# Kernel tuning notes

Hardware: AMD Instinct MI355X
Metric: run time of the kernel (lower is better)

The kernel has to match this reference:

```python
import jax, jax.numpy as jnp
import numpy as np

B, N, F = 1048576, 20, 7
RADIUS = 0.15
L1, L2 = 0.1, 2.0


def setup_inputs() -> dict:
    key = jax.random.key(0)
    ks = jax.random.split(key, 8)
    half = N // 2
    return {
        "x": jax.random.normal(ks[0], (B, N, F), dtype=jnp.float32),
        "W1": jax.random.normal(ks[1], (39, 64), dtype=jnp.float32) * 0.1,
        "b1": jax.random.normal(ks[2], (64,), dtype=jnp.float32) * 0.1,
        "W2": jax.random.normal(ks[3], (64, 64), dtype=jnp.float32) * 0.1,
        "b2": jax.random.normal(ks[4], (64,), dtype=jnp.float32) * 0.1,
        "W3": jax.random.normal(ks[5], (64, 5), dtype=jnp.float32) * 0.1,
        "b3": jax.random.normal(ks[6], (5,), dtype=jnp.float32) * 0.1,
        "idx": jax.random.randint(ks[7], (8,), 0, half, dtype=jnp.int32),
    }


def _build_observation(x, idx):
    # x: [B, N, 7]; agent_index = 0 (init kwarg)
    agent_index = 0
    half = N // 2
    Bsz = x.shape[0]
    pos = x[:, agent_index, 0:2]                      # [B,2]
    o_self = x[:, agent_index, 0:5]                   # [B,5]

    # three random agent neighbors: rel goal-like quantity, then a zero column
    xi = x[:, idx[0:3], :]                            # [B,3,7]
    rel = xi[..., 5:7] + xi[..., 0:2] - pos[:, None]  # [B,3,2]
    mid = jnp.concatenate(
        [rel, jnp.zeros((Bsz, 3, 1), dtype=x.dtype)], axis=2
    ).reshape(Bsz, 9)

    # five random obstacles (second half): distance-masked relative pos + features
    jdx = idx[3:8] + half
    xo = x[:, jdx, :]                                 # [B,5,7]
    d = xo[..., 0:2] - pos[:, None]                   # [B,5,2]
    dist = jnp.linalg.norm(d, axis=-1)                # [B,5]
    mask = (dist < RADIUS)[..., None]                 # [B,5,1]
    a = jnp.where(mask, d, 0.0)                       # [B,5,2]
    f = jnp.where(mask, xo[..., 2:5], 0.0)            # [B,5,3]
    obst = jnp.concatenate([a, f], axis=2).reshape(Bsz, 25)

    return jnp.concatenate([o_self, mid, obst], axis=1)  # [B,39]


def reference(x, W1, b1, W2, b2, W3, b3, idx):
    obs = _build_observation(x, idx)
    h = jax.nn.relu(obs @ W1 + b1)
    h = jax.nn.relu(h @ W2 + b2)
    r = h @ W3 + b3                                   # [B,5]
    res = jnp.stack([r[:, 1] - r[:, 2], r[:, 3] - r[:, 4]], axis=1) * L1
    res = jnp.where(jnp.abs(res) > 1.0, jnp.sign(res) * L2, res)
    return res
```

## Files before the change

### kernel.cpp

```cpp
#include <hip/hip_runtime.h>
#include <math.h>


#define NROW 20
#define NF   7
#define ITEM_F (NROW * NF)
#define BLOCK 128

__global__ __launch_bounds__(BLOCK) void maddpg_kernel(
    const float* __restrict__ x,
    const float* __restrict__ W1, const float* __restrict__ b1,
    const float* __restrict__ W2, const float* __restrict__ b2,
    const float* __restrict__ W3, const float* __restrict__ b3,
    const int*   __restrict__ idx,
    float2*      __restrict__ out,
    int nitems)
{
    __shared__ float buf[64 * BLOCK];

    const int tid = threadIdx.x;
    const long b  = (long)blockIdx.x * BLOCK + tid;
    if (b >= nitems) return;

    const float* xb = x + b * (long)ITEM_F;

    float4 s0 = *(const float4*)(xb);
    float  s4 = xb[4];
    const float px = s0.x, py = s0.y;
    buf[0*BLOCK + tid] = s0.x;
    buf[1*BLOCK + tid] = s0.y;
    buf[2*BLOCK + tid] = s0.z;
    buf[3*BLOCK + tid] = s0.w;
    buf[4*BLOCK + tid] = s4;

    #pragma unroll
    for (int t = 0; t < 3; t++) {
        const float* xr = xb + idx[t] * NF;
        float2 p01 = *(const float2*)(xr);
        float2 p56 = *(const float2*)(xr + 5);
        buf[(5 + 3*t + 0)*BLOCK + tid] = p56.x + p01.x - px;
        buf[(5 + 3*t + 1)*BLOCK + tid] = p56.y + p01.y - py;
        buf[(5 + 3*t + 2)*BLOCK + tid] = 0.0f;
    }

    #pragma unroll
    for (int t = 0; t < 5; t++) {
        const float* xr = xb + (idx[3 + t] + NROW/2) * NF;
        float4 q  = *(const float4*)(xr);
        float  q4 = xr[4];
        float dx = q.x - px, dy = q.y - py;
        bool  m  = sqrtf(dx*dx + dy*dy) < 0.15f;
        buf[(14 + 5*t + 0)*BLOCK + tid] = m ? dx  : 0.0f;
        buf[(14 + 5*t + 1)*BLOCK + tid] = m ? dy  : 0.0f;
        buf[(14 + 5*t + 2)*BLOCK + tid] = m ? q.z : 0.0f;
        buf[(14 + 5*t + 3)*BLOCK + tid] = m ? q.w : 0.0f;
        buf[(14 + 5*t + 4)*BLOCK + tid] = m ? q4  : 0.0f;
    }

    float h[64];
    #pragma unroll
    for (int k = 0; k < 64; k++) h[k] = b1[k];

    #pragma unroll 1
    for (int i = 0; i < 39; i++) {
        float o = buf[i*BLOCK + tid];
        const float* w = W1 + i * 64;
        #pragma unroll
        for (int k = 0; k < 64; k++) h[k] = fmaf(o, w[k], h[k]);
    }
    #pragma unroll
    for (int k = 0; k < 64; k++) buf[k*BLOCK + tid] = fmaxf(h[k], 0.0f);

    #pragma unroll
    for (int k = 0; k < 64; k++) h[k] = b2[k];

    #pragma unroll 1
    for (int i = 0; i < 64; i++) {
        float o = buf[i*BLOCK + tid];
        const float* w = W2 + i * 64;
        #pragma unroll
        for (int k = 0; k < 64; k++) h[k] = fmaf(o, w[k], h[k]);
    }
    #pragma unroll
    for (int k = 0; k < 64; k++) buf[k*BLOCK + tid] = fmaxf(h[k], 0.0f);

    float r1 = b3[1], r2 = b3[2], r3 = b3[3], r4 = b3[4];
    #pragma unroll 1
    for (int i = 0; i < 64; i++) {
        float o = buf[i*BLOCK + tid];
        const float* w = W3 + i * 5;
        r1 = fmaf(o, w[1], r1);
        r2 = fmaf(o, w[2], r2);
        r3 = fmaf(o, w[3], r3);
        r4 = fmaf(o, w[4], r4);
    }

    float v0 = (r1 - r2) * 0.1f;
    float v1 = (r3 - r4) * 0.1f;
    if (fabsf(v0) > 1.0f) v0 = copysignf(2.0f, v0);
    if (fabsf(v1) > 1.0f) v1 = copysignf(2.0f, v1);

    out[b] = make_float2(v0, v1);
}

extern "C" void kernel_launch(void* const* d_in, const int* in_sizes, int n_in,
                              void* d_out, int out_size, void* d_ws, size_t ws_size,
                              hipStream_t stream) {
    const float* x  = (const float*)d_in[0];
    const float* W1 = (const float*)d_in[1];
    const float* b1 = (const float*)d_in[2];
    const float* W2 = (const float*)d_in[3];
    const float* b2 = (const float*)d_in[4];
    const float* W3 = (const float*)d_in[5];
    const float* b3 = (const float*)d_in[6];
    const int*   idx = (const int*)d_in[7];
    float2* out = (float2*)d_out;

    int nitems = in_sizes[0] / ITEM_F;
    int grid = (nitems + BLOCK - 1) / BLOCK;
    maddpg_kernel<<<grid, BLOCK, 0, stream>>>(x, W1, b1, W2, b2, W3, b3, idx,
                                              out, nitems);
}
```

Before: 1.016 ms.

## Use packed FP32 FMAs in registers, drop LDS staging, skip masked obstacle rows

Removes the shared-memory staging buffer and keeps observations and hidden activations in registers. All three layers are fully unrolled and use two-wide packed FMA vectors. Obstacle rows of W1 are skipped for a whole wavefront when no lane's mask is set, and known-zero columns are dropped. Block size grows to 256 with a two-blocks occupancy hint, at the cost of much higher register pressure from full unrolling.

```diff
diff --git a/kernel.cpp b/kernel.cpp
--- a/kernel.cpp
+++ b/kernel.cpp
@@ -5,9 +5,21 @@
 #define NROW 20
 #define NF   7
 #define ITEM_F (NROW * NF)
-#define BLOCK 128
+#define BLOCK 256
 
-__global__ __launch_bounds__(BLOCK) void maddpg_kernel(
+typedef float v2 __attribute__((ext_vector_type(2)));
+
+__device__ __forceinline__ void row_fma(v2 (&h)[32], float o,
+                                        const float* __restrict__ wrow) {
+    const v2* w = (const v2*)wrow;
+    #pragma unroll
+    for (int k = 0; k < 32; k++) {
+        v2 ov; ov.x = o; ov.y = o;
+        h[k] = __builtin_elementwise_fma(ov, w[k], h[k]);
+    }
+}
+
+__global__ __launch_bounds__(BLOCK, 2) void maddpg_kernel(
     const float* __restrict__ x,
     const float* __restrict__ W1, const float* __restrict__ b1,
     const float* __restrict__ W2, const float* __restrict__ b2,
@@ -16,8 +28,6 @@
     float2*      __restrict__ out,
     int nitems)
 {
-    __shared__ float buf[64 * BLOCK];
-
     const int tid = threadIdx.x;
     const long b  = (long)blockIdx.x * BLOCK + tid;
     if (b >= nitems) return;
@@ -27,22 +37,19 @@
     float4 s0 = *(const float4*)(xb);
     float  s4 = xb[4];
     const float px = s0.x, py = s0.y;
-    buf[0*BLOCK + tid] = s0.x;
-    buf[1*BLOCK + tid] = s0.y;
-    buf[2*BLOCK + tid] = s0.z;
-    buf[3*BLOCK + tid] = s0.w;
-    buf[4*BLOCK + tid] = s4;
 
+    float mo[6];
     #pragma unroll
     for (int t = 0; t < 3; t++) {
         const float* xr = xb + idx[t] * NF;
         float2 p01 = *(const float2*)(xr);
         float2 p56 = *(const float2*)(xr + 5);
-        buf[(5 + 3*t + 0)*BLOCK + tid] = p56.x + p01.x - px;
-        buf[(5 + 3*t + 1)*BLOCK + tid] = p56.y + p01.y - py;
-        buf[(5 + 3*t + 2)*BLOCK + tid] = 0.0f;
+        mo[2*t + 0] = p56.x + p01.x - px;
+        mo[2*t + 1] = p56.y + p01.y - py;
     }
 
+    float oa[5][5];
+    int   anyt[5];
     #pragma unroll
     for (int t = 0; t < 5; t++) {
         const float* xr = xb + (idx[3 + t] + NROW/2) * NF;
@@ -50,53 +57,74 @@
         float  q4 = xr[4];
         float dx = q.x - px, dy = q.y - py;
         bool  m  = sqrtf(dx*dx + dy*dy) < 0.15f;
-        buf[(14 + 5*t + 0)*BLOCK + tid] = m ? dx  : 0.0f;
-        buf[(14 + 5*t + 1)*BLOCK + tid] = m ? dy  : 0.0f;
-        buf[(14 + 5*t + 2)*BLOCK + tid] = m ? q.z : 0.0f;
-        buf[(14 + 5*t + 3)*BLOCK + tid] = m ? q.w : 0.0f;
-        buf[(14 + 5*t + 4)*BLOCK + tid] = m ? q4  : 0.0f;
+        oa[t][0] = m ? dx  : 0.0f;
+        oa[t][1] = m ? dy  : 0.0f;
+        oa[t][2] = m ? q.z : 0.0f;
+        oa[t][3] = m ? q.w : 0.0f;
+        oa[t][4] = m ? q4  : 0.0f;
+        anyt[t]  = __any(m);
     }
 
-    float h[64];
+    v2 h[32];
+    const v2* b1v = (const v2*)b1;
     #pragma unroll
-    for (int k = 0; k < 64; k++) h[k] = b1[k];
+    for (int k = 0; k < 32; k++) h[k] = b1v[k];
 
-    #pragma unroll 1
-    for (int i = 0; i < 39; i++) {
-        float o = buf[i*BLOCK + tid];
-        const float* w = W1 + i * 64;
-        #pragma unroll
-        for (int k = 0; k < 64; k++) h[k] = fmaf(o, w[k], h[k]);
+    row_fma(h, s0.x, W1 + 0*64);
+    row_fma(h, s0.y, W1 + 1*64);
+    row_fma(h, s0.z, W1 + 2*64);
+    row_fma(h, s0.w, W1 + 3*64);
+    row_fma(h, s4,   W1 + 4*64);
+    #pragma unroll
+    for (int t = 0; t < 3; t++) {
+        row_fma(h, mo[2*t + 0], W1 + (5 + 3*t)*64);
+        row_fma(h, mo[2*t + 1], W1 + (6 + 3*t)*64);
     }
     #pragma unroll
-    for (int k = 0; k < 64; k++) buf[k*BLOCK + tid] = fmaxf(h[k], 0.0f);
+    for (int t = 0; t < 5; t++) {
+        if (anyt[t]) {
+            #pragma unroll
+            for (int j = 0; j < 5; j++)
+                row_fma(h, oa[t][j], W1 + (14 + 5*t + j)*64);
+        }
+    }
 
+    v2 a[32];
     #pragma unroll
-    for (int k = 0; k < 64; k++) h[k] = b2[k];
+    for (int k = 0; k < 32; k++) {
+        a[k].x = fmaxf(h[k].x, 0.0f);
+        a[k].y = fmaxf(h[k].y, 0.0f);
+    }
 
-    #pragma unroll 1
+    const v2* b2v = (const v2*)b2;
+    #pragma unroll
+    for (int k = 0; k < 32; k++) h[k] = b2v[k];
+    #pragma unroll
     for (int i = 0; i < 64; i++) {
-        float o = buf[i*BLOCK + tid];
-        const float* w = W2 + i * 64;
-        #pragma unroll
-        for (int k = 0; k < 64; k++) h[k] = fmaf(o, w[k], h[k]);
+        float o = (i & 1) ? a[i >> 1].y : a[i >> 1].x;
+        row_fma(h, o, W2 + i*64);
     }
     #pragma unroll
-    for (int k = 0; k < 64; k++) buf[k*BLOCK + tid] = fmaxf(h[k], 0.0f);
-
-    float r1 = b3[1], r2 = b3[2], r3 = b3[3], r4 = b3[4];
-    #pragma unroll 1
-    for (int i = 0; i < 64; i++) {
-        float o = buf[i*BLOCK + tid];
-        const float* w = W3 + i * 5;
-        r1 = fmaf(o, w[1], r1);
-        r2 = fmaf(o, w[2], r2);
-        r3 = fmaf(o, w[3], r3);
-        r4 = fmaf(o, w[4], r4);
+    for (int k = 0; k < 32; k++) {
+        a[k].x = fmaxf(h[k].x, 0.0f);
+        a[k].y = fmaxf(h[k].y, 0.0f);
     }
 
-    float v0 = (r1 - r2) * 0.1f;
-    float v1 = (r3 - r4) * 0.1f;
+    v2 rA; rA.x = b3[1]; rA.y = b3[2];
+    v2 rB; rB.x = b3[3]; rB.y = b3[4];
+    #pragma unroll
+    for (int i = 0; i < 64; i++) {
+        float o = (i & 1) ? a[i >> 1].y : a[i >> 1].x;
+        const float* w = W3 + i*5;
+        v2 ov; ov.x = o; ov.y = o;
+        v2 wA; wA.x = w[1]; wA.y = w[2];
+        v2 wB; wB.x = w[3]; wB.y = w[4];
+        rA = __builtin_elementwise_fma(ov, wA, rA);
+        rB = __builtin_elementwise_fma(ov, wB, rB);
+    }
+
+    float v0 = (rA.x - rA.y) * 0.1f;
+    float v1 = (rB.x - rB.y) * 0.1f;
     if (fabsf(v0) > 1.0f) v0 = copysignf(2.0f, v0);
     if (fabsf(v1) > 1.0f) v1 = copysignf(2.0f, v1);
 
```

Result: faster. 933.4 us (-8.2%).
